# Kernel optimization log

Measured on AMD Instinct MI355X. Metric: run time of the kernel, lower is better.

## Reference

```python
import jax, jax.numpy as jnp
import numpy as np

EPS = 1e-12  # matches torch F.normalize default eps


def _l2norm(x):
    # F.normalize(x, dim=-1): x / max(||x||, eps)
    n = jnp.sqrt(jnp.sum(x * x, axis=-1, keepdims=True))
    return x / jnp.maximum(n, EPS)


def setup_inputs() -> dict:
    key = jax.random.key(0)
    kq, kk, kv = jax.random.split(key, 3)
    B, H, N, D = 8, 16, 1024, 64
    q = jax.random.normal(kq, (B, H, N, D), dtype=jnp.float32)
    k = jax.random.normal(kk, (B, H, N, D), dtype=jnp.float32)
    v = jax.random.normal(kv, (B, H, N, D), dtype=jnp.float32)
    return {"q": q, "k": k, "v": v}


def reference(q, k, v):
    B, H, N, D = q.shape
    qn = _l2norm(q)  # [B,H,N,D]
    kn = _l2norm(k)  # [B,H,N,D]
    # cosine-similarity attention logits: [B,H,N,N]
    attn = jnp.einsum("bhnd,bhmd->bhnm", qn, kn)
    attn = jax.nn.softmax(attn, axis=-1)
    # attn_drop is identity (p=0)
    x = jnp.einsum("bhnm,bhmd->bhnd", attn, v)  # [B,H,N,D]
    # transpose(1,2).reshape(B, -1, H*D)
    x = jnp.transpose(x, (0, 2, 1, 3)).reshape(B, N, H * D)
    return x
```

## Files before the change

kernel.cpp:

```cpp
#include <hip/hip_runtime.h>
#include <stdint.h>

typedef __attribute__((ext_vector_type(8))) short short8;
typedef __attribute__((ext_vector_type(4))) float floatx4;

#define B_   8
#define H_   16
#define N_   1024
#define D_   64
#define NH_  (B_*H_)
#define LOG2E 1.44269504088896340736f
#define IMG_SHORTS 4096
#define NCHUNK 16

extern "C" {
__device__ float __ocml_native_exp2_f32(float);
__device__ float __ocml_native_rsqrt_f32(float);
}

__device__ __forceinline__ unsigned int pk2(float a, float b) {
    unsigned int ua = __float_as_uint(a) + 0x8000u;
    unsigned int ub = __float_as_uint(b) + 0x8000u;
    return __builtin_amdgcn_perm(ub, ua, 0x07060302);
}


__global__ __launch_bounds__(512) void prep_kv(
    const float* __restrict__ k, const float* __restrict__ v,
    unsigned short* __restrict__ kimg, unsigned short* __restrict__ vimg)
{
    const int bid = blockIdx.x;
    const int head = bid >> 4, ck = bid & 15;
    const int tid = threadIdx.x, w = tid >> 6, lane = tid & 63;

    const float* kh = k + (size_t)head * N_ * D_;
    const float* vh = v + (size_t)head * N_ * D_;
    unsigned short* kd = kimg + ((size_t)(head * 16 + ck)) * IMG_SHORTS;
    unsigned short* vd = vimg + ((size_t)(head * 16 + ck)) * IMG_SHORTS;

    const int srow = w * 8 + (lane >> 3);
    const int cbk  = lane & 7;
    const int ksw  = srow & 7;
    const float* kp = kh + ((size_t)(ck * 64 + srow)) * D_ + cbk * 8;
    float4 kx0 = *(const float4*)(kp);
    float4 kx1 = *(const float4*)(kp + 4);
    float ss = kx0.x*kx0.x + kx0.y*kx0.y + kx0.z*kx0.z + kx0.w*kx0.w
             + kx1.x*kx1.x + kx1.y*kx1.y + kx1.z*kx1.z + kx1.w*kx1.w;
    ss += __shfl_xor(ss, 1);
    ss += __shfl_xor(ss, 2);
    ss += __shfl_xor(ss, 4);
    float sc = __ocml_native_rsqrt_f32(ss);
    union { unsigned int u[4]; short8 s8; } pk;
    pk.u[0] = pk2(kx0.x*sc, kx0.y*sc); pk.u[1] = pk2(kx0.z*sc, kx0.w*sc);
    pk.u[2] = pk2(kx1.x*sc, kx1.y*sc); pk.u[3] = pk2(kx1.z*sc, kx1.w*sc);
    *(short8*)&kd[srow * 64 + ((cbk ^ ksw) << 3)] = pk.s8;

    const int Lb   = ((w >> 2) << 5) + ((w & 3) << 2);
    const int vwin = (w ^ (lane & 7)) << 3;
    float vr[8];
    #pragma unroll
    for (int j = 0; j < 8; j++) {
        int L = Lb + ((j >> 2) << 4) + (j & 3);
        vr[j] = vh[((size_t)(ck * 64 + L)) * D_ + lane];
    }
    union { unsigned int u[4]; short8 s8; } pv;
    pv.u[0] = pk2(vr[0], vr[1]); pv.u[1] = pk2(vr[2], vr[3]);
    pv.u[2] = pk2(vr[4], vr[5]); pv.u[3] = pk2(vr[6], vr[7]);
    *(short8*)&vd[lane * 64 + vwin] = pv.s8;
}

__global__ __launch_bounds__(512, 4) void attn_fused2(
    const float* __restrict__ q,
    const unsigned short* __restrict__ kimg,
    const unsigned short* __restrict__ vimg,
    float* __restrict__ out)
{
    __shared__ __align__(16) unsigned short ks[2][64 * 64];
    __shared__ __align__(16) unsigned short vt[2][64 * 64];

    const int bid = blockIdx.x;
    const int xcd = bid & 7, rest = bid >> 3;
    const int qt = rest & 3;
    const int head = (rest >> 2) * 8 + xcd;
    const int tid = threadIdx.x, w = tid >> 6, lane = tid & 63;
    const int lam = lane & 15, quad = lane >> 4;
    const int sw = lam & 7;
    const int q0 = qt * 256 + w * 32;

    const float* qh = q + ((size_t)head * N_ + q0) * D_;
    const unsigned short* kih = kimg + (size_t)head * 16 * IMG_SHORTS;
    const unsigned short* vih = vimg + (size_t)head * 16 * IMG_SHORTS;

    short8 aq[2][2];
    #pragma unroll
    for (int t = 0; t < 2; t++) {
        const float* qr = qh + (t * 16 + lam) * D_ + quad * 8;
        float4 f0 = *(const float4*)(qr);
        float4 f1 = *(const float4*)(qr + 4);
        float4 f2 = *(const float4*)(qr + 32);
        float4 f3 = *(const float4*)(qr + 36);
        float ss = f0.x*f0.x + f0.y*f0.y + f0.z*f0.z + f0.w*f0.w
                 + f1.x*f1.x + f1.y*f1.y + f1.z*f1.z + f1.w*f1.w
                 + f2.x*f2.x + f2.y*f2.y + f2.z*f2.z + f2.w*f2.w
                 + f3.x*f3.x + f3.y*f3.y + f3.z*f3.z + f3.w*f3.w;
        ss += __shfl_xor(ss, 16);
        ss += __shfl_xor(ss, 32);
        float sc = LOG2E * __ocml_native_rsqrt_f32(ss);
        union { unsigned int u[4]; short8 s8; } p0, p1;
        p0.u[0] = pk2(f0.x*sc, f0.y*sc); p0.u[1] = pk2(f0.z*sc, f0.w*sc);
        p0.u[2] = pk2(f1.x*sc, f1.y*sc); p0.u[3] = pk2(f1.z*sc, f1.w*sc);
        p1.u[0] = pk2(f2.x*sc, f2.y*sc); p1.u[1] = pk2(f2.z*sc, f2.w*sc);
        p1.u[2] = pk2(f3.x*sc, f3.y*sc); p1.u[3] = pk2(f3.z*sc, f3.w*sc);
        aq[t][0] = p0.s8; aq[t][1] = p1.s8;
    }

    floatx4 oacc[2][4];
    #pragma unroll
    for (int t = 0; t < 2; t++)
        #pragma unroll
        for (int dt = 0; dt < 4; dt++) oacc[t][dt] = (floatx4){0.f, 0.f, 0.f, 0.f};
    float l[2] = {0.f, 0.f};

    unsigned short* kw0 = &ks[0][w * 512];
    unsigned short* kw1 = &ks[1][w * 512];
    unsigned short* vw0 = &vt[0][w * 512];
    unsigned short* vw1 = &vt[1][w * 512];
    auto stage_dma = [&](int buf, int ck) {
        const unsigned short* kg = kih + ck * IMG_SHORTS + tid * 8;
        const unsigned short* vg = vih + ck * IMG_SHORTS + tid * 8;
        __builtin_amdgcn_global_load_lds(
            reinterpret_cast<const unsigned int*>(kg),
            reinterpret_cast<unsigned int*>(buf ? kw1 : kw0), 16, 0, 0);
        __builtin_amdgcn_global_load_lds(
            reinterpret_cast<const unsigned int*>(vg),
            reinterpret_cast<unsigned int*>(buf ? vw1 : vw0), 16, 0, 0);
    };

    auto compute = [&](int buf) {
        const unsigned short* ksb = &ks[buf][0];
        const unsigned short* vsb = &vt[buf][0];
        #pragma unroll
        for (int g = 0; g < 2; g++) {
            floatx4 s[2][2];
            #pragma unroll
            for (int s2 = 0; s2 < 2; s2++) {
                int st = g * 2 + s2;
                short8 bk0 = *(const short8*)(ksb + (st * 16 + lam) * 64 + (((0 + quad) ^ sw) << 3));
                short8 bk1 = *(const short8*)(ksb + (st * 16 + lam) * 64 + (((4 + quad) ^ sw) << 3));
                #pragma unroll
                for (int t = 0; t < 2; t++) {
                    floatx4 acc = (floatx4){0.f, 0.f, 0.f, 0.f};
                    acc = __builtin_amdgcn_mfma_f32_16x16x32_bf16(bk0, aq[t][0], acc, 0, 0, 0);
                    acc = __builtin_amdgcn_mfma_f32_16x16x32_bf16(bk1, aq[t][1], acc, 0, 0, 0);
                    s[t][s2] = acc;
                }
            }
            short8 pa[2];
            #pragma unroll
            for (int t = 0; t < 2; t++) {
                float e00 = __ocml_native_exp2_f32(s[t][0][0]);
                float e01 = __ocml_native_exp2_f32(s[t][0][1]);
                float e02 = __ocml_native_exp2_f32(s[t][0][2]);
                float e03 = __ocml_native_exp2_f32(s[t][0][3]);
                float e10 = __ocml_native_exp2_f32(s[t][1][0]);
                float e11 = __ocml_native_exp2_f32(s[t][1][1]);
                float e12 = __ocml_native_exp2_f32(s[t][1][2]);
                float e13 = __ocml_native_exp2_f32(s[t][1][3]);
                l[t] += ((e00 + e01) + (e02 + e03)) + ((e10 + e11) + (e12 + e13));
                union { unsigned int u[4]; short8 s8; } pk;
                pk.u[0] = pk2(e00, e01); pk.u[1] = pk2(e02, e03);
                pk.u[2] = pk2(e10, e11); pk.u[3] = pk2(e12, e13);
                pa[t] = pk.s8;
            }
            #pragma unroll
            for (int dt = 0; dt < 4; dt++) {
                short8 bv = *(const short8*)(vsb + (dt * 16 + lam) * 64 + (((g * 4 + quad) ^ sw) << 3));
                #pragma unroll
                for (int t = 0; t < 2; t++)
                    oacc[t][dt] = __builtin_amdgcn_mfma_f32_16x16x32_bf16(pa[t], bv, oacc[t][dt], 0, 0, 0);
            }
        }
    };

    stage_dma(0, 0);
    __syncthreads();
    for (int c = 0; c < 16; ++c) {
        int buf = c & 1;
        if (c < 15) stage_dma(buf ^ 1, c + 1);
        compute(buf);
        __syncthreads();
    }

    const int b = head >> 4, hh = head & 15;
    #pragma unroll
    for (int t = 0; t < 2; t++) {
        float lr = l[t];
        lr += __shfl_xor(lr, 16);
        lr += __shfl_xor(lr, 32);
        float rl = 1.0f / lr;
        float rq[4];
        #pragma unroll
        for (int r = 0; r < 4; r++) rq[r] = __shfl(rl, quad * 4 + r);
        float* ob = out + ((size_t)b * N_ + q0 + t * 16) * (H_ * D_) + hh * 64;
        #pragma unroll
        for (int dt = 0; dt < 4; dt++)
            #pragma unroll
            for (int r = 0; r < 4; r++)
                ob[(quad * 4 + r) * (H_ * D_) + dt * 16 + lam] = oacc[t][dt][r] * rq[r];
    }
}

__global__ __launch_bounds__(512, 4) void attn_fused(
    const float* __restrict__ q, const float* __restrict__ k,
    const float* __restrict__ v, float* __restrict__ out)
{
    __shared__ __align__(16) unsigned short ks[2][64 * 64];
    __shared__ __align__(16) unsigned short vt[2][64 * 64];

    const int bid = blockIdx.x;
    const int xcd = bid & 7, rest = bid >> 3;
    const int qt = rest & 3;
    const int head = (rest >> 2) * 8 + xcd;
    const int tid = threadIdx.x, w = tid >> 6, lane = tid & 63;
    const int lam = lane & 15, quad = lane >> 4;
    const int sw = lam & 7;
    const int q0 = qt * 256 + w * 32;

    const float* qh = q + ((size_t)head * N_ + q0) * D_;
    const float* kh = k + (size_t)head * N_ * D_;
    const float* vh = v + (size_t)head * N_ * D_;

    short8 aq[2][2];
    #pragma unroll
    for (int t = 0; t < 2; t++) {
        const float* qr = qh + (t * 16 + lam) * D_ + quad * 8;
        float4 f0 = *(const float4*)(qr);
        float4 f1 = *(const float4*)(qr + 4);
        float4 f2 = *(const float4*)(qr + 32);
        float4 f3 = *(const float4*)(qr + 36);
        float ss = f0.x*f0.x + f0.y*f0.y + f0.z*f0.z + f0.w*f0.w
                 + f1.x*f1.x + f1.y*f1.y + f1.z*f1.z + f1.w*f1.w
                 + f2.x*f2.x + f2.y*f2.y + f2.z*f2.z + f2.w*f2.w
                 + f3.x*f3.x + f3.y*f3.y + f3.z*f3.z + f3.w*f3.w;
        ss += __shfl_xor(ss, 16);
        ss += __shfl_xor(ss, 32);
        float sc = LOG2E * __ocml_native_rsqrt_f32(ss);
        union { unsigned int u[4]; short8 s8; } p0, p1;
        p0.u[0] = pk2(f0.x*sc, f0.y*sc); p0.u[1] = pk2(f0.z*sc, f0.w*sc);
        p0.u[2] = pk2(f1.x*sc, f1.y*sc); p0.u[3] = pk2(f1.z*sc, f1.w*sc);
        p1.u[0] = pk2(f2.x*sc, f2.y*sc); p1.u[1] = pk2(f2.z*sc, f2.w*sc);
        p1.u[2] = pk2(f3.x*sc, f3.y*sc); p1.u[3] = pk2(f3.z*sc, f3.w*sc);
        aq[t][0] = p0.s8; aq[t][1] = p1.s8;
    }

    floatx4 oacc[2][4];
    #pragma unroll
    for (int t = 0; t < 2; t++)
        #pragma unroll
        for (int dt = 0; dt < 4; dt++) oacc[t][dt] = (floatx4){0.f, 0.f, 0.f, 0.f};
    float l[2] = {0.f, 0.f};

    const int srow = w * 8 + (lane >> 3);
    const int cbk  = lane & 7;
    const int ksw  = srow & 7;
    const int Lb   = ((w >> 2) << 5) + ((w & 3) << 2);
    const int vwin = (w ^ (lane & 7)) << 3;

    float4 kx[2];
    float  vr[8];

    auto gload = [&](int ck) {
        const float* kp = kh + ((size_t)(ck * 64 + srow)) * D_ + cbk * 8;
        kx[0] = *(const float4*)(kp);
        kx[1] = *(const float4*)(kp + 4);
        #pragma unroll
        for (int j = 0; j < 8; j++) {
            int L = Lb + ((j >> 2) << 4) + (j & 3);
            vr[j] = vh[((size_t)(ck * 64 + L)) * D_ + lane];
        }
    };

    auto stage = [&](int buf) {
        float ss = kx[0].x*kx[0].x + kx[0].y*kx[0].y + kx[0].z*kx[0].z + kx[0].w*kx[0].w
                 + kx[1].x*kx[1].x + kx[1].y*kx[1].y + kx[1].z*kx[1].z + kx[1].w*kx[1].w;
        ss += __shfl_xor(ss, 1);
        ss += __shfl_xor(ss, 2);
        ss += __shfl_xor(ss, 4);
        float sc = __ocml_native_rsqrt_f32(ss);
        union { unsigned int u[4]; short8 s8; } pk;
        pk.u[0] = pk2(kx[0].x*sc, kx[0].y*sc); pk.u[1] = pk2(kx[0].z*sc, kx[0].w*sc);
        pk.u[2] = pk2(kx[1].x*sc, kx[1].y*sc); pk.u[3] = pk2(kx[1].z*sc, kx[1].w*sc);
        *(short8*)&ks[buf][srow * 64 + ((cbk ^ ksw) << 3)] = pk.s8;
        union { unsigned int u[4]; short8 s8; } pv;
        pv.u[0] = pk2(vr[0], vr[1]); pv.u[1] = pk2(vr[2], vr[3]);
        pv.u[2] = pk2(vr[4], vr[5]); pv.u[3] = pk2(vr[6], vr[7]);
        *(short8*)&vt[buf][lane * 64 + vwin] = pv.s8;
    };

    auto compute = [&](int buf) {
        const unsigned short* ksb = &ks[buf][0];
        const unsigned short* vsb = &vt[buf][0];
        #pragma unroll
        for (int g = 0; g < 2; g++) {
            floatx4 s[2][2];
            #pragma unroll
            for (int s2 = 0; s2 < 2; s2++) {
                int st = g * 2 + s2;
                short8 bk0 = *(const short8*)(ksb + (st * 16 + lam) * 64 + (((0 + quad) ^ sw) << 3));
                short8 bk1 = *(const short8*)(ksb + (st * 16 + lam) * 64 + (((4 + quad) ^ sw) << 3));
                #pragma unroll
                for (int t = 0; t < 2; t++) {
                    floatx4 acc = (floatx4){0.f, 0.f, 0.f, 0.f};
                    acc = __builtin_amdgcn_mfma_f32_16x16x32_bf16(bk0, aq[t][0], acc, 0, 0, 0);
                    acc = __builtin_amdgcn_mfma_f32_16x16x32_bf16(bk1, aq[t][1], acc, 0, 0, 0);
                    s[t][s2] = acc;
                }
            }
            short8 pa[2];
            #pragma unroll
            for (int t = 0; t < 2; t++) {
                float e00 = __ocml_native_exp2_f32(s[t][0][0]);
                float e01 = __ocml_native_exp2_f32(s[t][0][1]);
                float e02 = __ocml_native_exp2_f32(s[t][0][2]);
                float e03 = __ocml_native_exp2_f32(s[t][0][3]);
                float e10 = __ocml_native_exp2_f32(s[t][1][0]);
                float e11 = __ocml_native_exp2_f32(s[t][1][1]);
                float e12 = __ocml_native_exp2_f32(s[t][1][2]);
                float e13 = __ocml_native_exp2_f32(s[t][1][3]);
                l[t] += ((e00 + e01) + (e02 + e03)) + ((e10 + e11) + (e12 + e13));
                union { unsigned int u[4]; short8 s8; } pk;
                pk.u[0] = pk2(e00, e01); pk.u[1] = pk2(e02, e03);
                pk.u[2] = pk2(e10, e11); pk.u[3] = pk2(e12, e13);
                pa[t] = pk.s8;
            }
            #pragma unroll
            for (int dt = 0; dt < 4; dt++) {
                short8 bv = *(const short8*)(vsb + (dt * 16 + lam) * 64 + (((g * 4 + quad) ^ sw) << 3));
                #pragma unroll
                for (int t = 0; t < 2; t++)
                    oacc[t][dt] = __builtin_amdgcn_mfma_f32_16x16x32_bf16(pa[t], bv, oacc[t][dt], 0, 0, 0);
            }
        }
    };

    gload(0);
    stage(0);
    __syncthreads();
    for (int c = 0; c < 16; ++c) {
        int buf = c & 1;
        if (c < 15) gload(c + 1);
        compute(buf);
        if (c < 15) stage(buf ^ 1);
        __syncthreads();
    }

    const int b = head >> 4, hh = head & 15;
    #pragma unroll
    for (int t = 0; t < 2; t++) {
        float lr = l[t];
        lr += __shfl_xor(lr, 16);
        lr += __shfl_xor(lr, 32);
        float rl = 1.0f / lr;
        float rq[4];
        #pragma unroll
        for (int r = 0; r < 4; r++) rq[r] = __shfl(rl, quad * 4 + r);
        float* ob = out + ((size_t)b * N_ + q0 + t * 16) * (H_ * D_) + hh * 64;
        #pragma unroll
        for (int dt = 0; dt < 4; dt++)
            #pragma unroll
            for (int r = 0; r < 4; r++)
                ob[(quad * 4 + r) * (H_ * D_) + dt * 16 + lam] = oacc[t][dt][r] * rq[r];
    }
}

extern "C" void kernel_launch(void* const* d_in, const int* in_sizes, int n_in,
                              void* d_out, int out_size, void* d_ws, size_t ws_size,
                              hipStream_t stream) {
    const float* q = (const float*)d_in[0];
    const float* k = (const float*)d_in[1];
    const float* v = (const float*)d_in[2];
    float* out = (float*)d_out;
    const size_t need = (size_t)NH_ * NCHUNK * IMG_SHORTS * 2 * sizeof(unsigned short);
    if (d_ws != nullptr && ws_size >= need) {
        unsigned short* kimg = (unsigned short*)d_ws;
        unsigned short* vimg = kimg + (size_t)NH_ * NCHUNK * IMG_SHORTS;
        hipLaunchKernelGGL(prep_kv, dim3(NH_ * NCHUNK), dim3(512), 0, stream, k, v, kimg, vimg);
        hipLaunchKernelGGL(attn_fused2, dim3(NH_ * 4), dim3(512), 0, stream, q, kimg, vimg, out);
    } else {
        hipLaunchKernelGGL(attn_fused, dim3(NH_ * 4), dim3(512), 0, stream, q, k, v, out);
    }
}
```

Baseline: 165.7 us.

## Deepen K/V LDS pipeline to four buffers with prefetch distance two

Grows the K and V shared-memory rings from two to four buffers and prefetches two chunks ahead. Explicit vmcnt waits replace the per-iteration double syncthreads, leaving one barrier per chunk, so more DMA loads stay in flight while MFMA work runs. LDS use per block doubles to 64KB, which may cut the number of resident blocks per CU below the launch-bounds target. Correctness depends on the vmcnt counts matching the outstanding load_lds ops and on the four-buffer ring keeping writes clear of buffers still being read.

```diff
diff --git a/kernel.cpp b/kernel.cpp
--- a/kernel.cpp
+++ b/kernel.cpp
@@ -75,8 +75,8 @@
     const unsigned short* __restrict__ vimg,
     float* __restrict__ out)
 {
-    __shared__ __align__(16) unsigned short ks[2][64 * 64];
-    __shared__ __align__(16) unsigned short vt[2][64 * 64];
+    __shared__ __align__(16) unsigned short ks[4][64 * 64];
+    __shared__ __align__(16) unsigned short vt[4][64 * 64];
 
     const int bid = blockIdx.x;
     const int xcd = bid & 7, rest = bid >> 3;
@@ -121,24 +121,24 @@
         for (int dt = 0; dt < 4; dt++) oacc[t][dt] = (floatx4){0.f, 0.f, 0.f, 0.f};
     float l[2] = {0.f, 0.f};
 
-    unsigned short* kw0 = &ks[0][w * 512];
-    unsigned short* kw1 = &ks[1][w * 512];
-    unsigned short* vw0 = &vt[0][w * 512];
-    unsigned short* vw1 = &vt[1][w * 512];
+    unsigned short* ksbase = &ks[0][0];
+    unsigned short* vtbase = &vt[0][0];
     auto stage_dma = [&](int buf, int ck) {
         const unsigned short* kg = kih + ck * IMG_SHORTS + tid * 8;
         const unsigned short* vg = vih + ck * IMG_SHORTS + tid * 8;
+        unsigned short* kdst = ksbase + buf * IMG_SHORTS + w * 512;
+        unsigned short* vdst = vtbase + buf * IMG_SHORTS + w * 512;
         __builtin_amdgcn_global_load_lds(
             reinterpret_cast<const unsigned int*>(kg),
-            reinterpret_cast<unsigned int*>(buf ? kw1 : kw0), 16, 0, 0);
+            reinterpret_cast<unsigned int*>(kdst), 16, 0, 0);
         __builtin_amdgcn_global_load_lds(
             reinterpret_cast<const unsigned int*>(vg),
-            reinterpret_cast<unsigned int*>(buf ? vw1 : vw0), 16, 0, 0);
+            reinterpret_cast<unsigned int*>(vdst), 16, 0, 0);
     };
 
     auto compute = [&](int buf) {
-        const unsigned short* ksb = &ks[buf][0];
-        const unsigned short* vsb = &vt[buf][0];
+        const unsigned short* ksb = ksbase + buf * IMG_SHORTS;
+        const unsigned short* vsb = vtbase + buf * IMG_SHORTS;
         #pragma unroll
         for (int g = 0; g < 2; g++) {
             floatx4 s[2][2];
@@ -183,12 +183,19 @@
     };
 
     stage_dma(0, 0);
-    __syncthreads();
+    stage_dma(1, 1);
     for (int c = 0; c < 16; ++c) {
-        int buf = c & 1;
-        if (c < 15) stage_dma(buf ^ 1, c + 1);
-        compute(buf);
-        __syncthreads();
+        if (c < 14) {
+            stage_dma((c + 2) & 3, c + 2);
+            asm volatile("s_waitcnt vmcnt(4)" ::: "memory");
+        } else if (c == 14) {
+            asm volatile("s_waitcnt vmcnt(2)" ::: "memory");
+        } else {
+            asm volatile("s_waitcnt vmcnt(0)" ::: "memory");
+        }
+        __builtin_amdgcn_sched_barrier(0);
+        __builtin_amdgcn_s_barrier();
+        compute(c & 3);
     }
 
     const int b = head >> 4, hh = head & 15;
```

Result: no change. 164.4 us (-0.8%).
